# Performance work log

Measured on AMD Instinct MI355X. Metric: run time of the kernel, lower is better.

## Reference

```python
import jax, jax.numpy as jnp
import numpy as np

L, D, B, N, E, T = 3, 64, 1024, 131072, 1048576, 16
CH, HID = L * D, (L * D) // 2  # channel_dim=192, reduction=2 -> 96
BN_EPS = 1e-5


def setup_inputs() -> dict:
    key = jax.random.key(0)
    ks = jax.random.split(key, 20)
    rn = lambda k, sh, s=0.1: jax.random.normal(k, sh, jnp.float32) * s
    return {
        "query_x": rn(ks[0], (N, D), 1.0),
        "corpus_x": rn(ks[1], (N, D), 1.0),
        "query_edge_index": jax.random.randint(ks[2], (2, E), 0, N),
        "corpus_edge_index": jax.random.randint(ks[3], (2, E), 0, N),
        "query_graph_idx": jnp.sort(jax.random.randint(ks[4], (N,), 0, B)),
        "corpus_graph_idx": jnp.sort(jax.random.randint(ks[5], (N,), 0, B)),
        "gin_w1": rn(ks[6], (L, D, D)),
        "gin_b1": jnp.zeros((L, D), jnp.float32),
        "gin_w2": rn(ks[7], (L, D, D)),
        "gin_b2": jnp.zeros((L, D), jnp.float32),
        "bn_gamma": jnp.ones((L, D), jnp.float32),
        "bn_beta": jnp.zeros((L, D), jnp.float32),
        "gin_eps": jnp.zeros((L,), jnp.float32),
        "inner_w": rn(ks[8], (L, D, D)),
        "inner_b": jnp.zeros((L, D), jnp.float32),
        "outer_w": rn(ks[9], (L, D, D)),
        "outer_b": jnp.zeros((L, D), jnp.float32),
        "conv_w1": rn(ks[10], (CH, HID)),
        "conv_b1": jnp.zeros((HID,), jnp.float32),
        "conv_w2": rn(ks[11], (HID, HID)),
        "conv_b2": jnp.zeros((HID,), jnp.float32),
        "score_w1": rn(ks[12], (HID, 16)),
        "score_b1": jnp.zeros((16,), jnp.float32),
        "score_w2": rn(ks[13], (16, 1)),
        "score_b2": jnp.zeros((1,), jnp.float32),
        "ntn_w": rn(ks[14], (D, D, T), 0.05),
        "ntn_wb": rn(ks[15], (T, 2 * D), 0.05),
        "ntn_bias": jnp.zeros((T,), jnp.float32),
        "sim_w1": rn(ks[16], (T, T)),
        "sim_b1": jnp.zeros((T,), jnp.float32),
        "sim_w2": rn(ks[17], (T, 1)),
        "sim_b2": jnp.zeros((1,), jnp.float32),
        "alpha": jnp.ones((1,), jnp.float32),
        "beta": jnp.ones((1,), jnp.float32),
    }


def _encode(x, edge_index, graph_idx, p):
    """EncodingLayer: per layer GINConv -> ReLU -> inner MLP -> segment-sum pool -> outer MLP."""
    src, dst = edge_index[0], edge_index[1]
    feats = []
    for i in range(L):
        agg = jax.ops.segment_sum(x[src], dst, num_segments=N)  # neighbor sum (gather->scatter)
        h = (1.0 + p["gin_eps"][i]) * x + agg                    # GIN aggregation
        h = jax.nn.relu(h @ p["gin_w1"][i] + p["gin_b1"][i]) @ p["gin_w2"][i] + p["gin_b2"][i]
        mu = h.mean(axis=0)
        var = h.var(axis=0)
        h = (h - mu) * jax.lax.rsqrt(var + BN_EPS) * p["bn_gamma"][i] + p["bn_beta"][i]  # BatchNorm1d (train stats)
        x = jax.nn.relu(h)
        inner = jax.nn.relu(x @ p["inner_w"][i] + p["inner_b"][i])
        pooled = jax.ops.segment_sum(inner, graph_idx, num_segments=B)  # [B, D] graph pooling
        feats.append(jax.nn.relu(pooled @ p["outer_w"][i] + p["outer_b"][i]))
    return jnp.concatenate(feats, axis=1)  # [B, L*D]


def reference(query_x, corpus_x, query_edge_index, corpus_edge_index, query_graph_idx, corpus_graph_idx, gin_w1, gin_b1, gin_w2, gin_b2, bn_gamma, bn_beta, gin_eps, inner_w, inner_b, outer_w, outer_b, conv_w1, conv_b1, conv_w2, conv_b2, score_w1, score_b1, score_w2, score_b2, ntn_w, ntn_wb, ntn_bias, sim_w1, sim_b1, sim_w2, sim_b2, alpha, beta):
    p = {"gin_w1": gin_w1, "gin_b1": gin_b1, "gin_w2": gin_w2, "gin_b2": gin_b2,
         "bn_gamma": bn_gamma, "bn_beta": bn_beta, "gin_eps": gin_eps,
         "inner_w": inner_w, "inner_b": inner_b, "outer_w": outer_w, "outer_b": outer_b}
    qf = _encode(query_x, query_edge_index, query_graph_idx, p)   # [B, CH]
    cf = _encode(corpus_x, corpus_edge_index, corpus_graph_idx, p)
    # diff branch: conv_stack + score_layer
    diff = jnp.exp(-jnp.square(qf - cf))
    h = jax.nn.relu(diff @ conv_w1 + conv_b1)
    h = jnp.tanh(h @ conv_w2 + conv_b2)
    score = jax.nn.sigmoid(jax.nn.relu(h @ score_w1 + score_b1) @ score_w2 + score_b2)[:, 0]
    # NTN interaction branch on last-layer (filters[-1]) graph embeddings
    e1, e2 = qf[:, -D:], cf[:, -D:]
    scoring = jnp.einsum('bf,fgt,bg->bt', e1, ntn_w, e2)
    block = jnp.concatenate([e1, e2], axis=1) @ ntn_wb.T
    sim_rep = jax.nn.relu(scoring + block + ntn_bias)
    sim = jax.nn.sigmoid(jax.nn.relu(sim_rep @ sim_w1 + sim_b1) @ sim_w2 + sim_b2)[:, 0]
    return alpha[0] * score + beta[0] * sim  # [B]
```

## Files before the change

kernel.cpp:

```cpp
#include <hip/hip_runtime.h>
#include <hip/hip_bf16.h>

typedef __hip_bfloat16 bf16;
typedef __attribute__((ext_vector_type(8))) short short8;
typedef __attribute__((ext_vector_type(4))) float floatx4;

#define NN     131072
#define NEDGE  1048576
#define BG     1024
#define LAYERS 3
#define TG     8

__device__ __forceinline__ short f2bf_s(float f){
    union { float f; unsigned u; } x; x.f = f;
    unsigned r = x.u + 0x7fffu + ((x.u >> 16) & 1u);
    return (short)(r >> 16);
}
__device__ __forceinline__ float bf2f_s(short s){
    union { unsigned u; float f; } x; x.u = ((unsigned)(unsigned short)s) << 16;
    return x.f;
}
__device__ __forceinline__ void acc4(const unsigned short* p,
                                     float& a0, float& a1, float& a2, float& a3){
    ushort4 u = *(const ushort4*)p;
    a0 += bf2f_s((short)u.x); a1 += bf2f_s((short)u.y);
    a2 += bf2f_s((short)u.z); a3 += bf2f_s((short)u.w);
}

__global__ __launch_bounds__(256) void k_zero(int* __restrict__ cnt,
    const float* __restrict__ pooled_prev, const float* __restrict__ owp,
    const float* __restrict__ obp, float* __restrict__ feats_prev)
{
    int i = blockIdx.x*256 + threadIdx.x;
    if (i < NN) cnt[i] = 0;
    if (pooled_prev && blockIdx.x < 256) {
        int bb = i >> 6, j = i & 63;
        const float* pr = pooled_prev + bb*64;
        float a = obp[j];
        for (int k = 0; k < 64; k++) a = fmaf(pr[k], owp[k*64 + j], a);
        feats_prev[bb*192 + 128 + j] = fmaxf(a, 0.f);
    }
}

__global__ __launch_bounds__(256) void k_hist(const int* __restrict__ ei,
                                              int* __restrict__ cnt,
                                              int* __restrict__ rank)
{
    int e = blockIdx.x*256 + threadIdx.x;
    rank[e] = atomicAdd(cnt + ei[NEDGE + e], 1);
}

__global__ __launch_bounds__(256) void k_scan1(const int* __restrict__ cnt,
    int* __restrict__ rowptr, int* __restrict__ bsum)
{
    __shared__ int sd[256];
    int t = threadIdx.x;
    int base = blockIdx.x*1024 + t*4;
    int c0 = cnt[base], c1 = cnt[base+1], c2 = cnt[base+2], c3 = cnt[base+3];
    int tsum = c0 + c1 + c2 + c3;
    sd[t] = tsum;
    __syncthreads();
    for (int off = 1; off < 256; off <<= 1) {
        int v = (t >= off) ? sd[t-off] : 0;
        __syncthreads();
        sd[t] += v;
        __syncthreads();
    }
    int excl = sd[t] - tsum;
    rowptr[base]   = excl;
    rowptr[base+1] = excl + c0;
    rowptr[base+2] = excl + c0 + c1;
    rowptr[base+3] = excl + c0 + c1 + c2;
    if (t == 255) bsum[blockIdx.x] = sd[255];
}

__global__ __launch_bounds__(128) void k_scan2(const int* __restrict__ bsum,
    int* __restrict__ boff, int* __restrict__ rowptr)
{
    __shared__ int sd[128];
    int t = threadIdx.x;
    int v0 = bsum[t];
    sd[t] = v0;
    __syncthreads();
    for (int off = 1; off < 128; off <<= 1) {
        int v = (t >= off) ? sd[t-off] : 0;
        __syncthreads();
        sd[t] += v;
        __syncthreads();
    }
    boff[t] = sd[t] - v0;
    if (t == 0) rowptr[NN] = NEDGE;
}

__global__ __launch_bounds__(256) void k_scan3(int* __restrict__ rowptr,
    const int* __restrict__ boff)
{
    int i = blockIdx.x*256 + threadIdx.x;
    rowptr[i] += boff[i >> 10];
}

__global__ __launch_bounds__(256) void k_fill(const int* __restrict__ ei,
    const int* __restrict__ rowptr, const int* __restrict__ rank,
    int* __restrict__ col)
{
    int e = blockIdx.x*256 + threadIdx.x;
    int s = ei[e];
    int d = ei[NEDGE + e];
    col[rowptr[d] + rank[e]] = s;
}

__global__ __launch_bounds__(256) void k_cvt(const float* __restrict__ x,
                                             bf16* __restrict__ xh,
                                             float* __restrict__ zbuf)
{
    int i = blockIdx.x*256 + threadIdx.x;
    float4 v = ((const float4*)x)[i];
    short4 o;
    o.x = f2bf_s(v.x); o.y = f2bf_s(v.y);
    o.z = f2bf_s(v.z); o.w = f2bf_s(v.w);
    ((short4*)xh)[i] = o;
    if (i < 3*128 + 3*BG*64) zbuf[i] = 0.f;
}

__global__ __launch_bounds__(256) void k_wprep(
    const float* __restrict__ gw1, const float* __restrict__ gw2,
    const float* __restrict__ iw,
    short* __restrict__ w1h, short* __restrict__ w1l,
    short* __restrict__ w2h, short* __restrict__ w2l,
    short* __restrict__ wih, short* __restrict__ wil)
{
    int i = blockIdx.x*256 + threadIdx.x;
    if (i >= 3*LAYERS*4096) return;
    int msel = i / (LAYERS*4096);
    int rem  = i % (LAYERS*4096);
    int l = rem >> 12, idx = rem & 4095;
    int n = idx >> 6, k = idx & 63;
    const float* src = (msel==0) ? gw1 : (msel==1) ? gw2 : iw;
    float v = src[l*4096 + k*64 + n];
    short hi = f2bf_s(v);
    short lo = f2bf_s(v - bf2f_s(hi));
    short* dh = (msel==0) ? w1h : (msel==1) ? w2h : wih;
    short* dl = (msel==0) ? w1l : (msel==1) ? w2l : wil;
    dh[rem] = hi;
    dl[rem] = lo;
}

__global__ __launch_bounds__(256) void k_agg_gin(
    const bf16* __restrict__ xh,
    const int* __restrict__ rowptr, const int* __restrict__ col,
    const float* __restrict__ epsp,
    const short* __restrict__ w1h, const short* __restrict__ w1l,
    const float* __restrict__ b1,
    const short* __restrict__ w2h, const short* __restrict__ w2l,
    const float* __restrict__ b2,
    unsigned short* __restrict__ bigh, float* __restrict__ stats,
    const float* __restrict__ pooled_prev, const float* __restrict__ owp,
    const float* __restrict__ obp, float* __restrict__ feats, int coffp)
{
    __shared__ __align__(16) char buf[4][9472];
    __shared__ float red[2][4][64];
    int tid = threadIdx.x, wv = tid >> 6, lane = tid & 63;
    int q = lane >> 4, m = lane & 15;
    int nb = blockIdx.x*128 + wv*32;
    short* Sh = (short*)buf[wv];
    short* Sl = Sh + 2304;
    float ep = 1.0f + *epsp;

    if (pooled_prev && blockIdx.x < 256) {
        int g = blockIdx.x*256 + tid;
        int bb = g >> 6, j = g & 63;
        const float* pr = pooled_prev + bb*64;
        float a = obp[j];
        for (int k = 0; k < 64; k++) a = fmaf(pr[k], owp[k*64 + j], a);
        feats[bb*192 + coffp + j] = fmaxf(a, 0.f);
    }

    int gv = rowptr[nb + (lane < 33 ? lane : 32)];
    int fo = m * 4;
    const unsigned short* xt = (const unsigned short*)xh;

    for (int i = 0; i < 8; i++) {
        int row = i*4 + q;
        int rs = __shfl(gv, row, 64);
        int re = __shfl(gv, row+1, 64);
        float a0=0.f,a1=0.f,a2=0.f,a3=0.f;
        float e0=0.f,e1=0.f,e2=0.f,e3=0.f;
        float g0=0.f,g1=0.f,g2=0.f,g3=0.f;
        float h0=0.f,h1=0.f,h2=0.f,h3=0.f;
        int r = rs;
        for (; r + 4 <= re; r += 4) {
            int ca = col[r], cb = col[r+1], cc = col[r+2], cd = col[r+3];
            acc4(xt + (((size_t)ca) << 6) + fo, a0,a1,a2,a3);
            acc4(xt + (((size_t)cb) << 6) + fo, e0,e1,e2,e3);
            acc4(xt + (((size_t)cc) << 6) + fo, g0,g1,g2,g3);
            acc4(xt + (((size_t)cd) << 6) + fo, h0,h1,h2,h3);
        }
        for (; r < re; r++)
            acc4(xt + (((size_t)col[r]) << 6) + fo, a0,a1,a2,a3);
        a0 += e0 + g0 + h0;
        a1 += e1 + g1 + h1;
        a2 += e2 + g2 + h2;
        a3 += e3 + g3 + h3;
        ushort4 sv = *(const ushort4*)(xt + (((size_t)(nb+row)) << 6) + fo);
        a0 = fmaf(ep, bf2f_s((short)sv.x), a0);
        a1 = fmaf(ep, bf2f_s((short)sv.y), a1);
        a2 = fmaf(ep, bf2f_s((short)sv.z), a2);
        a3 = fmaf(ep, bf2f_s((short)sv.w), a3);
        short4 hh, ll;
        hh.x = f2bf_s(a0); ll.x = f2bf_s(a0 - bf2f_s(hh.x));
        hh.y = f2bf_s(a1); ll.y = f2bf_s(a1 - bf2f_s(hh.y));
        hh.z = f2bf_s(a2); ll.z = f2bf_s(a2 - bf2f_s(hh.z));
        hh.w = f2bf_s(a3); ll.w = f2bf_s(a3 - bf2f_s(hh.w));
        *(short4*)(Sh + row*72 + fo) = hh;
        *(short4*)(Sl + row*72 + fo) = ll;
    }
    __syncthreads();

    short8 Ah[2][2], Al[2][2];
    #pragma unroll
    for (int mc=0; mc<2; mc++)
      #pragma unroll
      for (int kc=0; kc<2; kc++){
        Ah[mc][kc] = *(const short8*)(Sh + (mc*16+m)*72 + kc*32 + q*8);
        Al[mc][kc] = *(const short8*)(Sl + (mc*16+m)*72 + kc*32 + q*8);
      }
    floatx4 acc[2][4];
    #pragma unroll
    for (int mc=0;mc<2;mc++)
      #pragma unroll
      for (int nc=0;nc<4;nc++) acc[mc][nc] = (floatx4){0.f,0.f,0.f,0.f};
    #pragma unroll
    for (int nc=0;nc<4;nc++){
      #pragma unroll
      for (int kc=0;kc<2;kc++){
        short8 bh = *(const short8*)(w1h + (nc*16+m)*64 + kc*32 + q*8);
        short8 bl = *(const short8*)(w1l + (nc*16+m)*64 + kc*32 + q*8);
        #pragma unroll
        for (int mc=0;mc<2;mc++){
          acc[mc][nc] = __builtin_amdgcn_mfma_f32_16x16x32_bf16(Ah[mc][kc], bh, acc[mc][nc],0,0,0);
          acc[mc][nc] = __builtin_amdgcn_mfma_f32_16x16x32_bf16(Al[mc][kc], bh, acc[mc][nc],0,0,0);
          acc[mc][nc] = __builtin_amdgcn_mfma_f32_16x16x32_bf16(Ah[mc][kc], bl, acc[mc][nc],0,0,0);
        }
      }
    }

    #pragma unroll
    for (int nc=0;nc<4;nc++){
      float bia = b1[nc*16+m];
      #pragma unroll
      for (int mc=0;mc<2;mc++)
        #pragma unroll
        for (int r=0;r<4;r++){
          float v = fmaxf(acc[mc][nc][r] + bia, 0.f);
          int row = mc*16 + q*4 + r, cl = nc*16 + m;
          short hb = f2bf_s(v);
          Sh[row*72+cl] = hb;
          Sl[row*72+cl] = f2bf_s(v - bf2f_s(hb));
        }
    }
    __syncthreads();

    short8 A2h[2][2], A2l[2][2];
    #pragma unroll
    for (int mc=0; mc<2; mc++)
      #pragma unroll
      for (int kc=0; kc<2; kc++){
        A2h[mc][kc] = *(const short8*)(Sh + (mc*16+m)*72 + kc*32 + q*8);
        A2l[mc][kc] = *(const short8*)(Sl + (mc*16+m)*72 + kc*32 + q*8);
      }
    floatx4 acc2[2][4];
    #pragma unroll
    for (int mc=0;mc<2;mc++)
      #pragma unroll
      for (int nc=0;nc<4;nc++) acc2[mc][nc] = (floatx4){0.f,0.f,0.f,0.f};
    #pragma unroll
    for (int nc=0;nc<4;nc++){
      #pragma unroll
      for (int kc=0;kc<2;kc++){
        short8 bh = *(const short8*)(w2h + (nc*16+m)*64 + kc*32 + q*8);
        short8 bl = *(const short8*)(w2l + (nc*16+m)*64 + kc*32 + q*8);
        #pragma unroll
        for (int mc=0;mc<2;mc++){
          acc2[mc][nc] = __builtin_amdgcn_mfma_f32_16x16x32_bf16(A2h[mc][kc], bh, acc2[mc][nc],0,0,0);
          acc2[mc][nc] = __builtin_amdgcn_mfma_f32_16x16x32_bf16(A2l[mc][kc], bh, acc2[mc][nc],0,0,0);
          acc2[mc][nc] = __builtin_amdgcn_mfma_f32_16x16x32_bf16(A2h[mc][kc], bl, acc2[mc][nc],0,0,0);
        }
      }
    }

    #pragma unroll
    for (int nc=0;nc<4;nc++){
      float bia = b2[nc*16+m];
      float s = 0.f, s2 = 0.f;
      #pragma unroll
      for (int mc=0;mc<2;mc++)
        #pragma unroll
        for (int r=0;r<4;r++){
          float v = acc2[mc][nc][r] + bia;
          bigh[(((size_t)(nb + mc*16 + q*4 + r)) << 6) + nc*16 + m] =
              (unsigned short)f2bf_s(v);
          s += v; s2 = fmaf(v, v, s2);
        }
      s  += __shfl_xor(s, 16, 64);  s  += __shfl_xor(s, 32, 64);
      s2 += __shfl_xor(s2,16, 64);  s2 += __shfl_xor(s2,32, 64);
      if (q == 0){ red[0][wv][nc*16+m] = s; red[1][wv][nc*16+m] = s2; }
    }
    __syncthreads();
    if (tid < 128){
      int which = tid >> 6, c = tid & 63;
      float a = red[which][0][c]+red[which][1][c]+red[which][2][c]+red[which][3][c];
      unsafeAtomicAdd(stats + which*64 + c, a);
    }
}

__global__ __launch_bounds__(256) void k_bn_inner(
    const unsigned short* __restrict__ bigh, const float* __restrict__ stats,
    const float* __restrict__ gam, const float* __restrict__ bet,
    const short* __restrict__ wih, const short* __restrict__ wil,
    const float* __restrict__ bi,
    bf16* __restrict__ xh,
    const int* __restrict__ gidx, float* __restrict__ pooled)
{
    __shared__ __align__(16) char buf[4][9472];
    int tid = threadIdx.x, wv = tid >> 6, lane = tid & 63;
    int q = lane >> 4, m = lane & 15;
    int nb = blockIdx.x*128 + wv*32;
    short* Sh = (short*)buf[wv];
    short* Sl = Sh + 2304;

    float mu  = stats[lane]    * (1.0f/NN);
    float ex2 = stats[64+lane] * (1.0f/NN);
    float var = ex2 - mu*mu;
    float sc  = gam[lane] * rsqrtf(var + 1e-5f);
    float sh  = bet[lane] - mu*sc;

    for (int rr = 0; rr < 32; rr++){
        float v = bf2f_s((short)bigh[(((size_t)(nb+rr)) << 6) + lane]);
        v = fmaxf(fmaf(v, sc, sh), 0.f);
        xh[(((size_t)(nb+rr)) << 6) + lane] = __float2bfloat16(v);
        short hb = f2bf_s(v);
        Sh[rr*72 + lane] = hb;
        Sl[rr*72 + lane] = f2bf_s(v - bf2f_s(hb));
    }
    __syncthreads();

    short8 A2h[2][2], A2l[2][2];
    #pragma unroll
    for (int mc=0; mc<2; mc++)
      #pragma unroll
      for (int kc=0; kc<2; kc++){
        A2h[mc][kc] = *(const short8*)(Sh + (mc*16+m)*72 + kc*32 + q*8);
        A2l[mc][kc] = *(const short8*)(Sl + (mc*16+m)*72 + kc*32 + q*8);
      }
    floatx4 acc[2][4];
    #pragma unroll
    for (int mc=0;mc<2;mc++)
      #pragma unroll
      for (int nc=0;nc<4;nc++) acc[mc][nc] = (floatx4){0.f,0.f,0.f,0.f};
    #pragma unroll
    for (int nc=0;nc<4;nc++){
      #pragma unroll
      for (int kc=0;kc<2;kc++){
        short8 bh = *(const short8*)(wih + (nc*16+m)*64 + kc*32 + q*8);
        short8 bl = *(const short8*)(wil + (nc*16+m)*64 + kc*32 + q*8);
        #pragma unroll
        for (int mc=0;mc<2;mc++){
          acc[mc][nc] = __builtin_amdgcn_mfma_f32_16x16x32_bf16(A2h[mc][kc], bh, acc[mc][nc],0,0,0);
          acc[mc][nc] = __builtin_amdgcn_mfma_f32_16x16x32_bf16(A2l[mc][kc], bh, acc[mc][nc],0,0,0);
          acc[mc][nc] = __builtin_amdgcn_mfma_f32_16x16x32_bf16(A2h[mc][kc], bl, acc[mc][nc],0,0,0);
        }
      }
    }
    __syncthreads();

    float* P = (float*)buf[wv];
    #pragma unroll
    for (int nc=0;nc<4;nc++){
      float bia = bi[nc*16+m];
      #pragma unroll
      for (int mc=0;mc<2;mc++)
        #pragma unroll
        for (int r=0;r<4;r++){
          float v = fmaxf(acc[mc][nc][r] + bia, 0.f);
          P[(mc*16 + q*4 + r)*66 + nc*16 + m] = v;
        }
    }
    __syncthreads();

    int gv = (lane < 32) ? gidx[nb + lane] : 0;
    int cur = __shfl(gv, 0, 64);
    float a = 0.f;
    for (int rr = 0; rr < 32; rr++){
        int g = __shfl(gv, rr, 64);
        if (g != cur){
            unsafeAtomicAdd(pooled + (size_t)cur*64 + lane, a);
            a = 0.f; cur = g;
        }
        a += P[rr*66 + lane];
    }
    unsafeAtomicAdd(pooled + (size_t)cur*64 + lane, a);
}

__global__ __launch_bounds__(256) void k_tail(
    const float* __restrict__ qf, const float* __restrict__ cf,
    const float* __restrict__ pooled_c2,
    const float* __restrict__ ow2, const float* __restrict__ ob2,
    const float* __restrict__ cw1, const float* __restrict__ cb1,
    const float* __restrict__ cw2, const float* __restrict__ cb2,
    const float* __restrict__ sw1, const float* __restrict__ sb1,
    const float* __restrict__ sw2, const float* __restrict__ sb2,
    const float* __restrict__ nw,  const float* __restrict__ nwb,
    const float* __restrict__ nb,
    const float* __restrict__ mw1, const float* __restrict__ mb1,
    const float* __restrict__ mw2, const float* __restrict__ mb2,
    const float* __restrict__ alpha, const float* __restrict__ beta,
    float* __restrict__ out)
{
    __shared__ float cws[192*96];
    __shared__ float diff[TG][192];
    __shared__ float e1s[TG][64], e2s[TG][64];
    __shared__ float h1s[TG][96], h2s[TG][96];
    __shared__ float s1s[TG][16], s2s[TG][16], srep[TG][16];
    __shared__ float red[16][16][TG];

    int t = threadIdx.x;
    int b0 = blockIdx.x * TG;

    {
        int b = t >> 5, o = (t & 31) * 2;
        const float* pr = pooled_c2 + (size_t)(b0 + b)*64;
        float a0 = ob2[o], a1 = ob2[o+1];
        for (int k = 0; k < 64; k++) {
            float p = pr[k];
            a0 = fmaf(p, ow2[k*64 + o], a0);
            a1 = fmaf(p, ow2[k*64 + o + 1], a1);
        }
        e2s[b][o]   = fmaxf(a0, 0.f);
        e2s[b][o+1] = fmaxf(a1, 0.f);
    }
    for (int i = t; i < 192*96; i += 256) cws[i] = cw1[i];
    __syncthreads();

    for (int i = t; i < TG*192; i += 256) {
        int b = i / 192, f = i % 192;
        float qv = qf[(b0+b)*192 + f];
        float cv = (f < 128) ? cf[(b0+b)*192 + f] : e2s[b][f-128];
        float d = qv - cv;
        diff[b][f] = __expf(-d*d);
        if (f >= 128) e1s[b][f-128] = qv;
    }
    __syncthreads();

    {
        int b = t >> 5, o = (t & 31) * 3;
        float a0 = cb1[o], a1 = cb1[o+1], a2 = cb1[o+2];
        for (int f = 0; f < 192; f++) {
            float d = diff[b][f];
            const float* w = cws + f*96 + o;
            a0 = fmaf(d, w[0], a0);
            a1 = fmaf(d, w[1], a1);
            a2 = fmaf(d, w[2], a2);
        }
        h1s[b][o] = fmaxf(a0, 0.f);
        h1s[b][o+1] = fmaxf(a1, 0.f);
        h1s[b][o+2] = fmaxf(a2, 0.f);
    }
    __syncthreads();
    for (int i = t; i < 96*96; i += 256) cws[i] = cw2[i];
    __syncthreads();
    {
        int b = t >> 5, o = (t & 31) * 3;
        float a0 = cb2[o], a1 = cb2[o+1], a2 = cb2[o+2];
        for (int f = 0; f < 96; f++) {
            float d = h1s[b][f];
            const float* w = cws + f*96 + o;
            a0 = fmaf(d, w[0], a0);
            a1 = fmaf(d, w[1], a1);
            a2 = fmaf(d, w[2], a2);
        }
        h2s[b][o] = tanhf(a0);
        h2s[b][o+1] = tanhf(a1);
        h2s[b][o+2] = tanhf(a2);
    }
    __syncthreads();
    if (t < TG*16) {
        int b = t >> 4, o = t & 15;
        float a = sb1[o];
        for (int f = 0; f < 96; f++) a = fmaf(h2s[b][f], sw1[f*16+o], a);
        s1s[b][o] = fmaxf(a, 0.f);
    }

    {
        int tt = t & 15, gq = t >> 4;
        int g0 = gq * 4;
        int lane = t & 63;
        float e1v[TG];
        #pragma unroll
        for (int b = 0; b < TG; b++) e1v[b] = e1s[b][lane];
        float v0[TG], v1[TG], v2[TG], v3[TG];
        #pragma unroll
        for (int b = 0; b < TG; b++) { v0[b]=0.f; v1[b]=0.f; v2[b]=0.f; v3[b]=0.f; }
        for (int f = 0; f < 64; f++) {
            const float* wp = nw + ((size_t)f*64 + g0)*16 + tt;
            float w0 = wp[0], w1 = wp[16], w2 = wp[32], w3 = wp[48];
            #pragma unroll
            for (int b = 0; b < TG; b++) {
                float e = __shfl(e1v[b], f, 64);
                v0[b] = fmaf(e, w0, v0[b]);
                v1[b] = fmaf(e, w1, v1[b]);
                v2[b] = fmaf(e, w2, v2[b]);
                v3[b] = fmaf(e, w3, v3[b]);
            }
        }
        #pragma unroll
        for (int b = 0; b < TG; b++) {
            float p = v0[b]*e2s[b][g0] + v1[b]*e2s[b][g0+1]
                    + v2[b]*e2s[b][g0+2] + v3[b]*e2s[b][g0+3];
            red[gq][tt][b] = p;
        }
    }
    __syncthreads();
    if (t < TG*16) {
        int b = t >> 4, tt = t & 15;
        float scv = 0.f;
        #pragma unroll
        for (int gq = 0; gq < 16; gq++) scv += red[gq][tt][b];
        float blk = nb[tt];
        for (int f = 0; f < 64; f++) blk = fmaf(e1s[b][f], nwb[tt*128 + f], blk);
        for (int f = 0; f < 64; f++) blk = fmaf(e2s[b][f], nwb[tt*128 + 64 + f], blk);
        srep[b][tt] = fmaxf(scv + blk, 0.f);
    }
    __syncthreads();
    if (t < TG*16) {
        int b = t >> 4, o = t & 15;
        float a = mb1[o];
        #pragma unroll
        for (int f = 0; f < 16; f++) a = fmaf(srep[b][f], mw1[f*16+o], a);
        s2s[b][o] = fmaxf(a, 0.f);
    }
    __syncthreads();
    if (t < TG) {
        float sco = sb2[0], sm = mb2[0];
        #pragma unroll
        for (int f = 0; f < 16; f++) {
            sco = fmaf(s1s[t][f], sw2[f], sco);
            sm  = fmaf(s2s[t][f], mw2[f], sm);
        }
        float score = 1.f / (1.f + __expf(-sco));
        float sim   = 1.f / (1.f + __expf(-sm));
        out[b0 + t] = alpha[0]*score + beta[0]*sim;
    }
}

extern "C" void kernel_launch(void* const* d_in, const int* in_sizes, int n_in,
                              void* d_out, int out_size, void* d_ws, size_t ws_size,
                              hipStream_t stream)
{
    const float* qx  = (const float*)d_in[0];
    const float* cx  = (const float*)d_in[1];
    const int*   qei = (const int*)d_in[2];
    const int*   cei = (const int*)d_in[3];
    const int*   qgi = (const int*)d_in[4];
    const int*   cgi = (const int*)d_in[5];
    const float* Wgw1 = (const float*)d_in[6];
    const float* Wgb1 = (const float*)d_in[7];
    const float* Wgw2 = (const float*)d_in[8];
    const float* Wgb2 = (const float*)d_in[9];
    const float* Wgam = (const float*)d_in[10];
    const float* Wbet = (const float*)d_in[11];
    const float* Weps = (const float*)d_in[12];
    const float* Wiw  = (const float*)d_in[13];
    const float* Wib  = (const float*)d_in[14];
    const float* Wow  = (const float*)d_in[15];
    const float* Wob  = (const float*)d_in[16];
    const float* Wcw1 = (const float*)d_in[17];
    const float* Wcb1 = (const float*)d_in[18];
    const float* Wcw2 = (const float*)d_in[19];
    const float* Wcb2 = (const float*)d_in[20];
    const float* Wsw1 = (const float*)d_in[21];
    const float* Wsb1 = (const float*)d_in[22];
    const float* Wsw2 = (const float*)d_in[23];
    const float* Wsb2 = (const float*)d_in[24];
    const float* Wnw  = (const float*)d_in[25];
    const float* Wnwb = (const float*)d_in[26];
    const float* Wnb  = (const float*)d_in[27];
    const float* Wmw1 = (const float*)d_in[28];
    const float* Wmb1 = (const float*)d_in[29];
    const float* Wmw2 = (const float*)d_in[30];
    const float* Wmb2 = (const float*)d_in[31];
    const float* Wal  = (const float*)d_in[32];
    const float* Wbe  = (const float*)d_in[33];

    float* F      = (float*)d_ws;
    float* big    = F;
    float* zbuf   = F + 8388608;
    float* stats3 = zbuf;
    float* pooled3= zbuf + 384;
    float* qf     = pooled3 + 3*BG*64;
    float* cf     = qf + 196608;
    int*   rowptr = (int*)(cf + 196608);
    int*   cnt    = rowptr + (NN + 1);
    int*   col    = cnt + NN;
    int*   bsum   = col + NEDGE;
    int*   boff   = bsum + 128;
    bf16*  xh     = (bf16*)(boff + 128);
    int*   rank   = (int*)big;
    unsigned short* bigh = (unsigned short*)big;
    uintptr_t wtb = (uintptr_t)(xh + (size_t)NN*64);
    wtb = (wtb + 63) & ~((uintptr_t)63);
    short* w1h = (short*)wtb;
    short* w1l = w1h + 3*4096;
    short* w2h = w1l + 3*4096;
    short* w2l = w2h + 3*4096;
    short* wih = w2l + 3*4096;
    short* wil = wih + 3*4096;

    k_wprep<<<144, 256, 0, stream>>>(Wgw1, Wgw2, Wiw, w1h, w1l, w2h, w2l, wih, wil);

    for (int side = 0; side < 2; side++) {
        const float* x0 = side ? cx  : qx;
        const int* ei   = side ? cei : qei;
        const int* gi   = side ? cgi : qgi;
        float* feats    = side ? cf  : qf;

        if (side == 0)
            k_zero<<<NN/256, 256, 0, stream>>>(cnt, nullptr, nullptr, nullptr, nullptr);
        else
            k_zero<<<NN/256, 256, 0, stream>>>(cnt, pooled3 + 2*BG*64,
                                               Wow + 2*4096, Wob + 2*64, qf);
        k_hist<<<NEDGE/256, 256, 0, stream>>>(ei, cnt, rank);
        k_scan1<<<128, 256, 0, stream>>>(cnt, rowptr, bsum);
        k_scan2<<<1, 128, 0, stream>>>(bsum, boff, rowptr);
        k_scan3<<<NN/256, 256, 0, stream>>>(rowptr, boff);
        k_fill<<<NEDGE/256, 256, 0, stream>>>(ei, rowptr, rank, col);

        k_cvt<<<NN*64/1024, 256, 0, stream>>>(x0, xh, zbuf);

        for (int l = 0; l < LAYERS; l++) {
            const float* pprev = (l == 0) ? nullptr : pooled3 + (size_t)(l-1)*BG*64;
            const float* owp   = (l == 0) ? nullptr : Wow + (l-1)*4096;
            const float* obp   = (l == 0) ? nullptr : Wob + (l-1)*64;
            k_agg_gin<<<NN/128, 256, 0, stream>>>(xh, rowptr, col, Weps + l,
                                                  w1h + l*4096, w1l + l*4096, Wgb1 + l*64,
                                                  w2h + l*4096, w2l + l*4096, Wgb2 + l*64,
                                                  bigh, stats3 + l*128,
                                                  pprev, owp, obp, feats, (l-1)*64);
            k_bn_inner<<<NN/128, 256, 0, stream>>>(bigh, stats3 + l*128,
                                                   Wgam + l*64, Wbet + l*64,
                                                   wih + l*4096, wil + l*4096,
                                                   Wib + l*64, xh, gi,
                                                   pooled3 + (size_t)l*BG*64);
        }
    }

    k_tail<<<BG/TG, 256, 0, stream>>>(qf, cf, pooled3 + 2*BG*64,
                                      Wow + 2*4096, Wob + 2*64,
                                      Wcw1, Wcb1, Wcw2, Wcb2,
                                      Wsw1, Wsb1, Wsw2, Wsb2,
                                      Wnw, Wnwb, Wnb, Wmw1, Wmb1, Wmw2, Wmb2,
                                      Wal, Wbe, (float*)d_out);
}
```

Measured before the change: 908.4 us.

## Merge query and corpus encoders into single batched kernel launches

Adds a merged path that processes the query and corpus graphs together. It builds one CSR over both graphs with offset node ids, and runs each GIN/BN/inner layer once with 2048 blocks instead of once per side. The outer-MLP epilogue for both sides is folded into the aggregation kernel, and the tail kernel takes both pooled buffers. The aim is to halve launch count and double grid size per launch to improve occupancy, at the cost of a larger workspace, and the path falls back to the old code if the workspace is too small.

```diff
diff --git a/kernel.cpp b/kernel.cpp
--- a/kernel.cpp
+++ b/kernel.cpp
@@ -10,6 +10,7 @@
 #define BG     1024
 #define LAYERS 3
 #define TG     8
+#define ZTOTM  (768 + 6*BG*64)
 
 __device__ __forceinline__ short f2bf_s(float f){
     union { float f; unsigned u; } x; x.f = f;
@@ -25,101 +26,6 @@
     ushort4 u = *(const ushort4*)p;
     a0 += bf2f_s((short)u.x); a1 += bf2f_s((short)u.y);
     a2 += bf2f_s((short)u.z); a3 += bf2f_s((short)u.w);
-}
-
-__global__ __launch_bounds__(256) void k_zero(int* __restrict__ cnt,
-    const float* __restrict__ pooled_prev, const float* __restrict__ owp,
-    const float* __restrict__ obp, float* __restrict__ feats_prev)
-{
-    int i = blockIdx.x*256 + threadIdx.x;
-    if (i < NN) cnt[i] = 0;
-    if (pooled_prev && blockIdx.x < 256) {
-        int bb = i >> 6, j = i & 63;
-        const float* pr = pooled_prev + bb*64;
-        float a = obp[j];
-        for (int k = 0; k < 64; k++) a = fmaf(pr[k], owp[k*64 + j], a);
-        feats_prev[bb*192 + 128 + j] = fmaxf(a, 0.f);
-    }
-}
-
-__global__ __launch_bounds__(256) void k_hist(const int* __restrict__ ei,
-                                              int* __restrict__ cnt,
-                                              int* __restrict__ rank)
-{
-    int e = blockIdx.x*256 + threadIdx.x;
-    rank[e] = atomicAdd(cnt + ei[NEDGE + e], 1);
-}
-
-__global__ __launch_bounds__(256) void k_scan1(const int* __restrict__ cnt,
-    int* __restrict__ rowptr, int* __restrict__ bsum)
-{
-    __shared__ int sd[256];
-    int t = threadIdx.x;
-    int base = blockIdx.x*1024 + t*4;
-    int c0 = cnt[base], c1 = cnt[base+1], c2 = cnt[base+2], c3 = cnt[base+3];
-    int tsum = c0 + c1 + c2 + c3;
-    sd[t] = tsum;
-    __syncthreads();
-    for (int off = 1; off < 256; off <<= 1) {
-        int v = (t >= off) ? sd[t-off] : 0;
-        __syncthreads();
-        sd[t] += v;
-        __syncthreads();
-    }
-    int excl = sd[t] - tsum;
-    rowptr[base]   = excl;
-    rowptr[base+1] = excl + c0;
-    rowptr[base+2] = excl + c0 + c1;
-    rowptr[base+3] = excl + c0 + c1 + c2;
-    if (t == 255) bsum[blockIdx.x] = sd[255];
-}
-
-__global__ __launch_bounds__(128) void k_scan2(const int* __restrict__ bsum,
-    int* __restrict__ boff, int* __restrict__ rowptr)
-{
-    __shared__ int sd[128];
-    int t = threadIdx.x;
-    int v0 = bsum[t];
-    sd[t] = v0;
-    __syncthreads();
-    for (int off = 1; off < 128; off <<= 1) {
-        int v = (t >= off) ? sd[t-off] : 0;
-        __syncthreads();
-        sd[t] += v;
-        __syncthreads();
-    }
-    boff[t] = sd[t] - v0;
-    if (t == 0) rowptr[NN] = NEDGE;
-}
-
-__global__ __launch_bounds__(256) void k_scan3(int* __restrict__ rowptr,
-    const int* __restrict__ boff)
-{
-    int i = blockIdx.x*256 + threadIdx.x;
-    rowptr[i] += boff[i >> 10];
-}
-
-__global__ __launch_bounds__(256) void k_fill(const int* __restrict__ ei,
-    const int* __restrict__ rowptr, const int* __restrict__ rank,
-    int* __restrict__ col)
-{
-    int e = blockIdx.x*256 + threadIdx.x;
-    int s = ei[e];
-    int d = ei[NEDGE + e];
-    col[rowptr[d] + rank[e]] = s;
-}
-
-__global__ __launch_bounds__(256) void k_cvt(const float* __restrict__ x,
-                                             bf16* __restrict__ xh,
-                                             float* __restrict__ zbuf)
-{
-    int i = blockIdx.x*256 + threadIdx.x;
-    float4 v = ((const float4*)x)[i];
-    short4 o;
-    o.x = f2bf_s(v.x); o.y = f2bf_s(v.y);
-    o.z = f2bf_s(v.z); o.w = f2bf_s(v.w);
-    ((short4*)xh)[i] = o;
-    if (i < 3*128 + 3*BG*64) zbuf[i] = 0.f;
 }
 
 __global__ __launch_bounds__(256) void k_wprep(
@@ -143,6 +49,616 @@
     short* dl = (msel==0) ? w1l : (msel==1) ? w2l : wil;
     dh[rem] = hi;
     dl[rem] = lo;
+}
+
+__global__ __launch_bounds__(256) void k_cvtM(const float* __restrict__ qx,
+                                              const float* __restrict__ cx,
+                                              bf16* __restrict__ xh,
+                                              int* __restrict__ cnt,
+                                              float* __restrict__ zbuf)
+{
+    int i = blockIdx.x*256 + threadIdx.x;
+    float4 v = (i < NN*16) ? ((const float4*)qx)[i]
+                           : ((const float4*)cx)[i - NN*16];
+    short4 o;
+    o.x = f2bf_s(v.x); o.y = f2bf_s(v.y);
+    o.z = f2bf_s(v.z); o.w = f2bf_s(v.w);
+    ((short4*)xh)[i] = o;
+    if (i < 2*NN)   cnt[i]  = 0;
+    if (i < ZTOTM)  zbuf[i] = 0.f;
+}
+
+__global__ __launch_bounds__(256) void k_histM(const int* __restrict__ qei,
+                                               const int* __restrict__ cei,
+                                               int* __restrict__ cnt,
+                                               int* __restrict__ rank)
+{
+    int e = blockIdx.x*256 + threadIdx.x;
+    int side = e >> 20;
+    int el = e & (NEDGE-1);
+    const int* ei = side ? cei : qei;
+    rank[e] = atomicAdd(cnt + ei[NEDGE + el] + side*NN, 1);
+}
+
+__global__ __launch_bounds__(256) void k_scan1M(const int* __restrict__ cnt,
+    int* __restrict__ rowptr, int* __restrict__ bsum)
+{
+    __shared__ int sd[256];
+    int t = threadIdx.x;
+    int base = blockIdx.x*1024 + t*4;
+    int c0 = cnt[base], c1 = cnt[base+1], c2 = cnt[base+2], c3 = cnt[base+3];
+    int tsum = c0 + c1 + c2 + c3;
+    sd[t] = tsum;
+    __syncthreads();
+    for (int off = 1; off < 256; off <<= 1) {
+        int v = (t >= off) ? sd[t-off] : 0;
+        __syncthreads();
+        sd[t] += v;
+        __syncthreads();
+    }
+    int excl = sd[t] - tsum;
+    rowptr[base]   = excl;
+    rowptr[base+1] = excl + c0;
+    rowptr[base+2] = excl + c0 + c1;
+    rowptr[base+3] = excl + c0 + c1 + c2;
+    if (t == 255) bsum[blockIdx.x] = sd[255];
+}
+
+__global__ __launch_bounds__(256) void k_scan2M(const int* __restrict__ bsum,
+    int* __restrict__ boff, int* __restrict__ rowptr)
+{
+    __shared__ int sd[256];
+    int t = threadIdx.x;
+    int v0 = bsum[t];
+    sd[t] = v0;
+    __syncthreads();
+    for (int off = 1; off < 256; off <<= 1) {
+        int v = (t >= off) ? sd[t-off] : 0;
+        __syncthreads();
+        sd[t] += v;
+        __syncthreads();
+    }
+    boff[t] = sd[t] - v0;
+    if (t == 0) rowptr[2*NN] = 2*NEDGE;
+}
+
+__global__ __launch_bounds__(256) void k_scan3M(int* __restrict__ rowptr,
+    const int* __restrict__ boff)
+{
+    int i = blockIdx.x*256 + threadIdx.x;
+    rowptr[i] += boff[i >> 10];
+}
+
+__global__ __launch_bounds__(256) void k_fillM(const int* __restrict__ qei,
+    const int* __restrict__ cei,
+    const int* __restrict__ rowptr, const int* __restrict__ rank,
+    int* __restrict__ col)
+{
+    int e = blockIdx.x*256 + threadIdx.x;
+    int side = e >> 20;
+    int el = e & (NEDGE-1);
+    const int* ei = side ? cei : qei;
+    int s = ei[el] + side*NN;
+    int d = ei[NEDGE + el] + side*NN;
+    col[rowptr[d] + rank[e]] = s;
+}
+
+__global__ __launch_bounds__(256) void k_agg_ginM(
+    const bf16* __restrict__ xh,
+    const int* __restrict__ rowptr, const int* __restrict__ col,
+    const float* __restrict__ epsp,
+    const short* __restrict__ w1h, const short* __restrict__ w1l,
+    const float* __restrict__ b1,
+    const short* __restrict__ w2h, const short* __restrict__ w2l,
+    const float* __restrict__ b2,
+    unsigned short* __restrict__ bigh, float* __restrict__ stats,
+    const float* __restrict__ pprev_q, const float* __restrict__ pprev_c,
+    const float* __restrict__ owp, const float* __restrict__ obp,
+    float* __restrict__ qf, float* __restrict__ cf, int coffp)
+{
+    __shared__ __align__(16) char buf[4][9472];
+    __shared__ float red[2][4][64];
+    int bid = blockIdx.x;
+    int side = bid >> 10;
+    int lb = bid & 1023;
+    int tid = threadIdx.x, wv = tid >> 6, lane = tid & 63;
+    int q = lane >> 4, m = lane & 15;
+    int nb = bid*128 + wv*32;
+    short* Sh = (short*)buf[wv];
+    short* Sl = Sh + 2304;
+    float ep = 1.0f + *epsp;
+
+    if (owp && lb < 256) {
+        int g = lb*256 + tid;
+        int bb = g >> 6, j = g & 63;
+        const float* pr = (side ? pprev_c : pprev_q) + bb*64;
+        float a = obp[j];
+        for (int k = 0; k < 64; k++) a = fmaf(pr[k], owp[k*64 + j], a);
+        float* feats = side ? cf : qf;
+        feats[bb*192 + coffp + j] = fmaxf(a, 0.f);
+    }
+
+    int gv = rowptr[nb + (lane < 33 ? lane : 32)];
+    int fo = m * 4;
+    const unsigned short* xt = (const unsigned short*)xh;
+
+    for (int i = 0; i < 8; i++) {
+        int row = i*4 + q;
+        int rs = __shfl(gv, row, 64);
+        int re = __shfl(gv, row+1, 64);
+        float a0=0.f,a1=0.f,a2=0.f,a3=0.f;
+        float e0=0.f,e1=0.f,e2=0.f,e3=0.f;
+        float g0=0.f,g1=0.f,g2=0.f,g3=0.f;
+        float h0=0.f,h1=0.f,h2=0.f,h3=0.f;
+        int r = rs;
+        for (; r + 4 <= re; r += 4) {
+            int ca = col[r], cb = col[r+1], cc = col[r+2], cd = col[r+3];
+            acc4(xt + (((size_t)ca) << 6) + fo, a0,a1,a2,a3);
+            acc4(xt + (((size_t)cb) << 6) + fo, e0,e1,e2,e3);
+            acc4(xt + (((size_t)cc) << 6) + fo, g0,g1,g2,g3);
+            acc4(xt + (((size_t)cd) << 6) + fo, h0,h1,h2,h3);
+        }
+        for (; r < re; r++)
+            acc4(xt + (((size_t)col[r]) << 6) + fo, a0,a1,a2,a3);
+        a0 += e0 + g0 + h0;
+        a1 += e1 + g1 + h1;
+        a2 += e2 + g2 + h2;
+        a3 += e3 + g3 + h3;
+        ushort4 sv = *(const ushort4*)(xt + (((size_t)(nb+row)) << 6) + fo);
+        a0 = fmaf(ep, bf2f_s((short)sv.x), a0);
+        a1 = fmaf(ep, bf2f_s((short)sv.y), a1);
+        a2 = fmaf(ep, bf2f_s((short)sv.z), a2);
+        a3 = fmaf(ep, bf2f_s((short)sv.w), a3);
+        short4 hh, ll;
+        hh.x = f2bf_s(a0); ll.x = f2bf_s(a0 - bf2f_s(hh.x));
+        hh.y = f2bf_s(a1); ll.y = f2bf_s(a1 - bf2f_s(hh.y));
+        hh.z = f2bf_s(a2); ll.z = f2bf_s(a2 - bf2f_s(hh.z));
+        hh.w = f2bf_s(a3); ll.w = f2bf_s(a3 - bf2f_s(hh.w));
+        *(short4*)(Sh + row*72 + fo) = hh;
+        *(short4*)(Sl + row*72 + fo) = ll;
+    }
+    __syncthreads();
+
+    short8 Ah[2][2], Al[2][2];
+    #pragma unroll
+    for (int mc=0; mc<2; mc++)
+      #pragma unroll
+      for (int kc=0; kc<2; kc++){
+        Ah[mc][kc] = *(const short8*)(Sh + (mc*16+m)*72 + kc*32 + q*8);
+        Al[mc][kc] = *(const short8*)(Sl + (mc*16+m)*72 + kc*32 + q*8);
+      }
+    floatx4 acc[2][4];
+    #pragma unroll
+    for (int mc=0;mc<2;mc++)
+      #pragma unroll
+      for (int nc=0;nc<4;nc++) acc[mc][nc] = (floatx4){0.f,0.f,0.f,0.f};
+    #pragma unroll
+    for (int nc=0;nc<4;nc++){
+      #pragma unroll
+      for (int kc=0;kc<2;kc++){
+        short8 bh = *(const short8*)(w1h + (nc*16+m)*64 + kc*32 + q*8);
+        short8 bl = *(const short8*)(w1l + (nc*16+m)*64 + kc*32 + q*8);
+        #pragma unroll
+        for (int mc=0;mc<2;mc++){
+          acc[mc][nc] = __builtin_amdgcn_mfma_f32_16x16x32_bf16(Ah[mc][kc], bh, acc[mc][nc],0,0,0);
+          acc[mc][nc] = __builtin_amdgcn_mfma_f32_16x16x32_bf16(Al[mc][kc], bh, acc[mc][nc],0,0,0);
+          acc[mc][nc] = __builtin_amdgcn_mfma_f32_16x16x32_bf16(Ah[mc][kc], bl, acc[mc][nc],0,0,0);
+        }
+      }
+    }
+
+    #pragma unroll
+    for (int nc=0;nc<4;nc++){
+      float bia = b1[nc*16+m];
+      #pragma unroll
+      for (int mc=0;mc<2;mc++)
+        #pragma unroll
+        for (int r=0;r<4;r++){
+          float v = fmaxf(acc[mc][nc][r] + bia, 0.f);
+          int row = mc*16 + q*4 + r, cl = nc*16 + m;
+          short hb = f2bf_s(v);
+          Sh[row*72+cl] = hb;
+          Sl[row*72+cl] = f2bf_s(v - bf2f_s(hb));
+        }
+    }
+    __syncthreads();
+
+    short8 A2h[2][2], A2l[2][2];
+    #pragma unroll
+    for (int mc=0; mc<2; mc++)
+      #pragma unroll
+      for (int kc=0; kc<2; kc++){
+        A2h[mc][kc] = *(const short8*)(Sh + (mc*16+m)*72 + kc*32 + q*8);
+        A2l[mc][kc] = *(const short8*)(Sl + (mc*16+m)*72 + kc*32 + q*8);
+      }
+    floatx4 acc2[2][4];
+    #pragma unroll
+    for (int mc=0;mc<2;mc++)
+      #pragma unroll
+      for (int nc=0;nc<4;nc++) acc2[mc][nc] = (floatx4){0.f,0.f,0.f,0.f};
+    #pragma unroll
+    for (int nc=0;nc<4;nc++){
+      #pragma unroll
+      for (int kc=0;kc<2;kc++){
+        short8 bh = *(const short8*)(w2h + (nc*16+m)*64 + kc*32 + q*8);
+        short8 bl = *(const short8*)(w2l + (nc*16+m)*64 + kc*32 + q*8);
+        #pragma unroll
+        for (int mc=0;mc<2;mc++){
+          acc2[mc][nc] = __builtin_amdgcn_mfma_f32_16x16x32_bf16(A2h[mc][kc], bh, acc2[mc][nc],0,0,0);
+          acc2[mc][nc] = __builtin_amdgcn_mfma_f32_16x16x32_bf16(A2l[mc][kc], bh, acc2[mc][nc],0,0,0);
+          acc2[mc][nc] = __builtin_amdgcn_mfma_f32_16x16x32_bf16(A2h[mc][kc], bl, acc2[mc][nc],0,0,0);
+        }
+      }
+    }
+
+    #pragma unroll
+    for (int nc=0;nc<4;nc++){
+      float bia = b2[nc*16+m];
+      float s = 0.f, s2 = 0.f;
+      #pragma unroll
+      for (int mc=0;mc<2;mc++)
+        #pragma unroll
+        for (int r=0;r<4;r++){
+          float v = acc2[mc][nc][r] + bia;
+          bigh[(((size_t)(nb + mc*16 + q*4 + r)) << 6) + nc*16 + m] =
+              (unsigned short)f2bf_s(v);
+          s += v; s2 = fmaf(v, v, s2);
+        }
+      s  += __shfl_xor(s, 16, 64);  s  += __shfl_xor(s, 32, 64);
+      s2 += __shfl_xor(s2,16, 64);  s2 += __shfl_xor(s2,32, 64);
+      if (q == 0){ red[0][wv][nc*16+m] = s; red[1][wv][nc*16+m] = s2; }
+    }
+    __syncthreads();
+    if (tid < 128){
+      int which = tid >> 6, c = tid & 63;
+      float a = red[which][0][c]+red[which][1][c]+red[which][2][c]+red[which][3][c];
+      unsafeAtomicAdd(stats + side*128 + which*64 + c, a);
+    }
+}
+
+__global__ __launch_bounds__(256) void k_bn_innerM(
+    const unsigned short* __restrict__ bigh, const float* __restrict__ stats,
+    const float* __restrict__ gam, const float* __restrict__ bet,
+    const short* __restrict__ wih, const short* __restrict__ wil,
+    const float* __restrict__ bi,
+    bf16* __restrict__ xh,
+    const int* __restrict__ gidx_q, const int* __restrict__ gidx_c,
+    float* __restrict__ pooled_q, float* __restrict__ pooled_c)
+{
+    __shared__ __align__(16) char buf[4][9472];
+    int bid = blockIdx.x;
+    int side = bid >> 10;
+    int tid = threadIdx.x, wv = tid >> 6, lane = tid & 63;
+    int q = lane >> 4, m = lane & 15;
+    int nb = bid*128 + wv*32;
+    short* Sh = (short*)buf[wv];
+    short* Sl = Sh + 2304;
+
+    const float* st = stats + side*128;
+    float mu  = st[lane]    * (1.0f/NN);
+    float ex2 = st[64+lane] * (1.0f/NN);
+    float var = ex2 - mu*mu;
+    float sc  = gam[lane] * rsqrtf(var + 1e-5f);
+    float sh  = bet[lane] - mu*sc;
+
+    for (int rr = 0; rr < 32; rr++){
+        float v = bf2f_s((short)bigh[(((size_t)(nb+rr)) << 6) + lane]);
+        v = fmaxf(fmaf(v, sc, sh), 0.f);
+        xh[(((size_t)(nb+rr)) << 6) + lane] = __float2bfloat16(v);
+        short hb = f2bf_s(v);
+        Sh[rr*72 + lane] = hb;
+        Sl[rr*72 + lane] = f2bf_s(v - bf2f_s(hb));
+    }
+    __syncthreads();
+
+    short8 A2h[2][2], A2l[2][2];
+    #pragma unroll
+    for (int mc=0; mc<2; mc++)
+      #pragma unroll
+      for (int kc=0; kc<2; kc++){
+        A2h[mc][kc] = *(const short8*)(Sh + (mc*16+m)*72 + kc*32 + q*8);
+        A2l[mc][kc] = *(const short8*)(Sl + (mc*16+m)*72 + kc*32 + q*8);
+      }
+    floatx4 acc[2][4];
+    #pragma unroll
+    for (int mc=0;mc<2;mc++)
+      #pragma unroll
+      for (int nc=0;nc<4;nc++) acc[mc][nc] = (floatx4){0.f,0.f,0.f,0.f};
+    #pragma unroll
+    for (int nc=0;nc<4;nc++){
+      #pragma unroll
+      for (int kc=0;kc<2;kc++){
+        short8 bh = *(const short8*)(wih + (nc*16+m)*64 + kc*32 + q*8);
+        short8 bl = *(const short8*)(wil + (nc*16+m)*64 + kc*32 + q*8);
+        #pragma unroll
+        for (int mc=0;mc<2;mc++){
+          acc[mc][nc] = __builtin_amdgcn_mfma_f32_16x16x32_bf16(A2h[mc][kc], bh, acc[mc][nc],0,0,0);
+          acc[mc][nc] = __builtin_amdgcn_mfma_f32_16x16x32_bf16(A2l[mc][kc], bh, acc[mc][nc],0,0,0);
+          acc[mc][nc] = __builtin_amdgcn_mfma_f32_16x16x32_bf16(A2h[mc][kc], bl, acc[mc][nc],0,0,0);
+        }
+      }
+    }
+    __syncthreads();
+
+    float* P = (float*)buf[wv];
+    #pragma unroll
+    for (int nc=0;nc<4;nc++){
+      float bia = bi[nc*16+m];
+      #pragma unroll
+      for (int mc=0;mc<2;mc++)
+        #pragma unroll
+        for (int r=0;r<4;r++){
+          float v = fmaxf(acc[mc][nc][r] + bia, 0.f);
+          P[(mc*16 + q*4 + r)*66 + nc*16 + m] = v;
+        }
+    }
+    __syncthreads();
+
+    const int* gidx = side ? gidx_c : gidx_q;
+    float* pooled   = side ? pooled_c : pooled_q;
+    int ln = nb - side*NN;
+    int gv = (lane < 32) ? gidx[ln + lane] : 0;
+    int cur = __shfl(gv, 0, 64);
+    float a = 0.f;
+    for (int rr = 0; rr < 32; rr++){
+        int g = __shfl(gv, rr, 64);
+        if (g != cur){
+            unsafeAtomicAdd(pooled + (size_t)cur*64 + lane, a);
+            a = 0.f; cur = g;
+        }
+        a += P[rr*66 + lane];
+    }
+    unsafeAtomicAdd(pooled + (size_t)cur*64 + lane, a);
+}
+
+__global__ __launch_bounds__(256) void k_tailM(
+    const float* __restrict__ qf, const float* __restrict__ cf,
+    const float* __restrict__ pooled_q2, const float* __restrict__ pooled_c2,
+    const float* __restrict__ ow2, const float* __restrict__ ob2,
+    const float* __restrict__ cw1, const float* __restrict__ cb1,
+    const float* __restrict__ cw2, const float* __restrict__ cb2,
+    const float* __restrict__ sw1, const float* __restrict__ sb1,
+    const float* __restrict__ sw2, const float* __restrict__ sb2,
+    const float* __restrict__ nw,  const float* __restrict__ nwb,
+    const float* __restrict__ nb,
+    const float* __restrict__ mw1, const float* __restrict__ mb1,
+    const float* __restrict__ mw2, const float* __restrict__ mb2,
+    const float* __restrict__ alpha, const float* __restrict__ beta,
+    float* __restrict__ out)
+{
+    __shared__ float cws[192*96];
+    __shared__ float diff[TG][192];
+    __shared__ float e1s[TG][64], e2s[TG][64];
+    __shared__ float h1s[TG][96], h2s[TG][96];
+    __shared__ float s1s[TG][16], s2s[TG][16], srep[TG][16];
+    __shared__ float red[16][16][TG];
+
+    int t = threadIdx.x;
+    int b0 = blockIdx.x * TG;
+
+    {
+        int b = t >> 5, o = (t & 31) * 2;
+        const float* prq = pooled_q2 + (size_t)(b0 + b)*64;
+        const float* prc = pooled_c2 + (size_t)(b0 + b)*64;
+        float q0 = ob2[o], q1 = ob2[o+1];
+        float c0 = ob2[o], c1 = ob2[o+1];
+        for (int k = 0; k < 64; k++) {
+            float w0 = ow2[k*64 + o], w1 = ow2[k*64 + o + 1];
+            float pq = prq[k], pc = prc[k];
+            q0 = fmaf(pq, w0, q0); q1 = fmaf(pq, w1, q1);
+            c0 = fmaf(pc, w0, c0); c1 = fmaf(pc, w1, c1);
+        }
+        e1s[b][o]   = fmaxf(q0, 0.f);
+        e1s[b][o+1] = fmaxf(q1, 0.f);
+        e2s[b][o]   = fmaxf(c0, 0.f);
+        e2s[b][o+1] = fmaxf(c1, 0.f);
+    }
+    for (int i = t; i < 192*96; i += 256) cws[i] = cw1[i];
+    __syncthreads();
+
+    for (int i = t; i < TG*192; i += 256) {
+        int b = i / 192, f = i % 192;
+        float qv = (f < 128) ? qf[(b0+b)*192 + f] : e1s[b][f-128];
+        float cv = (f < 128) ? cf[(b0+b)*192 + f] : e2s[b][f-128];
+        float d = qv - cv;
+        diff[b][f] = __expf(-d*d);
+    }
+    __syncthreads();
+
+    {
+        int b = t >> 5, o = (t & 31) * 3;
+        float a0 = cb1[o], a1 = cb1[o+1], a2 = cb1[o+2];
+        for (int f = 0; f < 192; f++) {
+            float d = diff[b][f];
+            const float* w = cws + f*96 + o;
+            a0 = fmaf(d, w[0], a0);
+            a1 = fmaf(d, w[1], a1);
+            a2 = fmaf(d, w[2], a2);
+        }
+        h1s[b][o] = fmaxf(a0, 0.f);
+        h1s[b][o+1] = fmaxf(a1, 0.f);
+        h1s[b][o+2] = fmaxf(a2, 0.f);
+    }
+    __syncthreads();
+    for (int i = t; i < 96*96; i += 256) cws[i] = cw2[i];
+    __syncthreads();
+    {
+        int b = t >> 5, o = (t & 31) * 3;
+        float a0 = cb2[o], a1 = cb2[o+1], a2 = cb2[o+2];
+        for (int f = 0; f < 96; f++) {
+            float d = h1s[b][f];
+            const float* w = cws + f*96 + o;
+            a0 = fmaf(d, w[0], a0);
+            a1 = fmaf(d, w[1], a1);
+            a2 = fmaf(d, w[2], a2);
+        }
+        h2s[b][o] = tanhf(a0);
+        h2s[b][o+1] = tanhf(a1);
+        h2s[b][o+2] = tanhf(a2);
+    }
+    __syncthreads();
+    if (t < TG*16) {
+        int b = t >> 4, o = t & 15;
+        float a = sb1[o];
+        for (int f = 0; f < 96; f++) a = fmaf(h2s[b][f], sw1[f*16+o], a);
+        s1s[b][o] = fmaxf(a, 0.f);
+    }
+
+    {
+        int tt = t & 15, gq = t >> 4;
+        int g0 = gq * 4;
+        int lane = t & 63;
+        float e1v[TG];
+        #pragma unroll
+        for (int b = 0; b < TG; b++) e1v[b] = e1s[b][lane];
+        float v0[TG], v1[TG], v2[TG], v3[TG];
+        #pragma unroll
+        for (int b = 0; b < TG; b++) { v0[b]=0.f; v1[b]=0.f; v2[b]=0.f; v3[b]=0.f; }
+        for (int f = 0; f < 64; f++) {
+            const float* wp = nw + ((size_t)f*64 + g0)*16 + tt;
+            float w0 = wp[0], w1 = wp[16], w2 = wp[32], w3 = wp[48];
+            #pragma unroll
+            for (int b = 0; b < TG; b++) {
+                float e = __shfl(e1v[b], f, 64);
+                v0[b] = fmaf(e, w0, v0[b]);
+                v1[b] = fmaf(e, w1, v1[b]);
+                v2[b] = fmaf(e, w2, v2[b]);
+                v3[b] = fmaf(e, w3, v3[b]);
+            }
+        }
+        #pragma unroll
+        for (int b = 0; b < TG; b++) {
+            float p = v0[b]*e2s[b][g0] + v1[b]*e2s[b][g0+1]
+                    + v2[b]*e2s[b][g0+2] + v3[b]*e2s[b][g0+3];
+            red[gq][tt][b] = p;
+        }
+    }
+    __syncthreads();
+    if (t < TG*16) {
+        int b = t >> 4, tt = t & 15;
+        float scv = 0.f;
+        #pragma unroll
+        for (int gq = 0; gq < 16; gq++) scv += red[gq][tt][b];
+        float blk = nb[tt];
+        for (int f = 0; f < 64; f++) blk = fmaf(e1s[b][f], nwb[tt*128 + f], blk);
+        for (int f = 0; f < 64; f++) blk = fmaf(e2s[b][f], nwb[tt*128 + 64 + f], blk);
+        srep[b][tt] = fmaxf(scv + blk, 0.f);
+    }
+    __syncthreads();
+    if (t < TG*16) {
+        int b = t >> 4, o = t & 15;
+        float a = mb1[o];
+        #pragma unroll
+        for (int f = 0; f < 16; f++) a = fmaf(srep[b][f], mw1[f*16+o], a);
+        s2s[b][o] = fmaxf(a, 0.f);
+    }
+    __syncthreads();
+    if (t < TG) {
+        float sco = sb2[0], sm = mb2[0];
+        #pragma unroll
+        for (int f = 0; f < 16; f++) {
+            sco = fmaf(s1s[t][f], sw2[f], sco);
+            sm  = fmaf(s2s[t][f], mw2[f], sm);
+        }
+        float score = 1.f / (1.f + __expf(-sco));
+        float sim   = 1.f / (1.f + __expf(-sm));
+        out[b0 + t] = alpha[0]*score + beta[0]*sim;
+    }
+}
+
+__global__ __launch_bounds__(256) void k_zero(int* __restrict__ cnt,
+    const float* __restrict__ pooled_prev, const float* __restrict__ owp,
+    const float* __restrict__ obp, float* __restrict__ feats_prev)
+{
+    int i = blockIdx.x*256 + threadIdx.x;
+    if (i < NN) cnt[i] = 0;
+    if (pooled_prev && blockIdx.x < 256) {
+        int bb = i >> 6, j = i & 63;
+        const float* pr = pooled_prev + bb*64;
+        float a = obp[j];
+        for (int k = 0; k < 64; k++) a = fmaf(pr[k], owp[k*64 + j], a);
+        feats_prev[bb*192 + 128 + j] = fmaxf(a, 0.f);
+    }
+}
+
+__global__ __launch_bounds__(256) void k_hist(const int* __restrict__ ei,
+                                              int* __restrict__ cnt,
+                                              int* __restrict__ rank)
+{
+    int e = blockIdx.x*256 + threadIdx.x;
+    rank[e] = atomicAdd(cnt + ei[NEDGE + e], 1);
+}
+
+__global__ __launch_bounds__(256) void k_scan1(const int* __restrict__ cnt,
+    int* __restrict__ rowptr, int* __restrict__ bsum)
+{
+    __shared__ int sd[256];
+    int t = threadIdx.x;
+    int base = blockIdx.x*1024 + t*4;
+    int c0 = cnt[base], c1 = cnt[base+1], c2 = cnt[base+2], c3 = cnt[base+3];
+    int tsum = c0 + c1 + c2 + c3;
+    sd[t] = tsum;
+    __syncthreads();
+    for (int off = 1; off < 256; off <<= 1) {
+        int v = (t >= off) ? sd[t-off] : 0;
+        __syncthreads();
+        sd[t] += v;
+        __syncthreads();
+    }
+    int excl = sd[t] - tsum;
+    rowptr[base]   = excl;
+    rowptr[base+1] = excl + c0;
+    rowptr[base+2] = excl + c0 + c1;
+    rowptr[base+3] = excl + c0 + c1 + c2;
+    if (t == 255) bsum[blockIdx.x] = sd[255];
+}
+
+__global__ __launch_bounds__(128) void k_scan2(const int* __restrict__ bsum,
+    int* __restrict__ boff, int* __restrict__ rowptr)
+{
+    __shared__ int sd[128];
+    int t = threadIdx.x;
+    int v0 = bsum[t];
+    sd[t] = v0;
+    __syncthreads();
+    for (int off = 1; off < 128; off <<= 1) {
+        int v = (t >= off) ? sd[t-off] : 0;
+        __syncthreads();
+        sd[t] += v;
+        __syncthreads();
+    }
+    boff[t] = sd[t] - v0;
+    if (t == 0) rowptr[NN] = NEDGE;
+}
+
+__global__ __launch_bounds__(256) void k_scan3(int* __restrict__ rowptr,
+    const int* __restrict__ boff)
+{
+    int i = blockIdx.x*256 + threadIdx.x;
+    rowptr[i] += boff[i >> 10];
+}
+
+__global__ __launch_bounds__(256) void k_fill(const int* __restrict__ ei,
+    const int* __restrict__ rowptr, const int* __restrict__ rank,
+    int* __restrict__ col)
+{
+    int e = blockIdx.x*256 + threadIdx.x;
+    int s = ei[e];
+    int d = ei[NEDGE + e];
+    col[rowptr[d] + rank[e]] = s;
+}
+
+__global__ __launch_bounds__(256) void k_cvt(const float* __restrict__ x,
+                                             bf16* __restrict__ xh,
+                                             float* __restrict__ zbuf)
+{
+    int i = blockIdx.x*256 + threadIdx.x;
+    float4 v = ((const float4*)x)[i];
+    short4 o;
+    o.x = f2bf_s(v.x); o.y = f2bf_s(v.y);
+    o.z = f2bf_s(v.z); o.w = f2bf_s(v.w);
+    ((short4*)xh)[i] = o;
+    if (i < 3*128 + 3*BG*64) zbuf[i] = 0.f;
 }
 
 __global__ __launch_bounds__(256) void k_agg_gin(
@@ -591,8 +1107,73 @@
     const float* Wal  = (const float*)d_in[32];
     const float* Wbe  = (const float*)d_in[33];
 
-    float* F      = (float*)d_ws;
-    float* big    = F;
+    float* F = (float*)d_ws;
+
+    const size_t MERGED_NEED = 86ull << 20;
+
+    if (ws_size >= MERGED_NEED) {
+        unsigned short* bigh = (unsigned short*)F;
+        int*   rank   = (int*)F;
+        bf16*  xh     = (bf16*)(F + 8388608);
+        float* zbuf   = F + 16777216;
+        float* stats3 = zbuf;
+        float* pooled3= zbuf + 768;
+        float* qf     = F + 16777216 + ZTOTM;
+        float* cf     = qf + 196608;
+        int*   rowptr = (int*)(cf + 196608);
+        int*   cnt    = rowptr + (2*NN + 1);
+        int*   col    = cnt + 2*NN;
+        int*   bsum   = col + 2*NEDGE;
+        int*   boff   = bsum + 256;
+        uintptr_t wtb = (uintptr_t)(boff + 256);
+        wtb = (wtb + 63) & ~((uintptr_t)63);
+        short* w1h = (short*)wtb;
+        short* w1l = w1h + 3*4096;
+        short* w2h = w1l + 3*4096;
+        short* w2l = w2h + 3*4096;
+        short* wih = w2l + 3*4096;
+        short* wil = wih + 3*4096;
+
+        k_wprep<<<144, 256, 0, stream>>>(Wgw1, Wgw2, Wiw, w1h, w1l, w2h, w2l, wih, wil);
+        k_cvtM  <<<16384, 256, 0, stream>>>(qx, cx, xh, cnt, zbuf);
+        k_histM <<<8192, 256, 0, stream>>>(qei, cei, cnt, rank);
+        k_scan1M<<<256, 256, 0, stream>>>(cnt, rowptr, bsum);
+        k_scan2M<<<1, 256, 0, stream>>>(bsum, boff, rowptr);
+        k_scan3M<<<1024, 256, 0, stream>>>(rowptr, boff);
+        k_fillM <<<8192, 256, 0, stream>>>(qei, cei, rowptr, rank, col);
+
+        for (int l = 0; l < LAYERS; l++) {
+            const float* ppq = (l == 0) ? nullptr : pooled3 + (size_t)(l-1)*BG*64;
+            const float* ppc = (l == 0) ? nullptr : pooled3 + (size_t)(3 + l-1)*BG*64;
+            const float* owp = (l == 0) ? nullptr : Wow + (l-1)*4096;
+            const float* obp = (l == 0) ? nullptr : Wob + (l-1)*64;
+            k_agg_ginM<<<2048, 256, 0, stream>>>(xh, rowptr, col, Weps + l,
+                                                 w1h + l*4096, w1l + l*4096, Wgb1 + l*64,
+                                                 w2h + l*4096, w2l + l*4096, Wgb2 + l*64,
+                                                 bigh, stats3 + l*256,
+                                                 ppq, ppc, owp, obp,
+                                                 qf, cf, (l-1)*64);
+            k_bn_innerM<<<2048, 256, 0, stream>>>(bigh, stats3 + l*256,
+                                                  Wgam + l*64, Wbet + l*64,
+                                                  wih + l*4096, wil + l*4096,
+                                                  Wib + l*64, xh, qgi, cgi,
+                                                  pooled3 + (size_t)l*BG*64,
+                                                  pooled3 + (size_t)(3 + l)*BG*64);
+        }
+
+        k_tailM<<<BG/TG, 256, 0, stream>>>(qf, cf,
+                                           pooled3 + (size_t)2*BG*64,
+                                           pooled3 + (size_t)5*BG*64,
+                                           Wow + 2*4096, Wob + 2*64,
+                                           Wcw1, Wcb1, Wcw2, Wcb2,
+                                           Wsw1, Wsb1, Wsw2, Wsb2,
+                                           Wnw, Wnwb, Wnb, Wmw1, Wmb1, Wmw2, Wmb2,
+                                           Wal, Wbe, (float*)d_out);
+        return;
+    }
+
+    unsigned short* bigh = (unsigned short*)F;
+    int*   rank   = (int*)F;
     float* zbuf   = F + 8388608;
     float* stats3 = zbuf;
     float* pooled3= zbuf + 384;
@@ -604,8 +1185,6 @@
     int*   bsum   = col + NEDGE;
     int*   boff   = bsum + 128;
     bf16*  xh     = (bf16*)(boff + 128);
-    int*   rank   = (int*)big;
-    unsigned short* bigh = (unsigned short*)big;
     uintptr_t wtb = (uintptr_t)(xh + (size_t)NN*64);
     wtb = (wtb + 63) & ~((uintptr_t)63);
     short* w1h = (short*)wtb;
```

After: 819.5 us. 1.11x faster.
